# Performance work log

Hardware: AMD Instinct MI355X
Metric: run time of the kernel (lower is better)

The kernel has to match this reference:

```python
import jax, jax.numpy as jnp
import numpy as np

N = 100000        # num nodes
E = 3_200_000     # num edges
NFEAT, NHID, NCLASS = 256, 128, 40
BN_EPS = 1e-5


def _gcn_norm(edge_index, edge_weight, num_nodes):
    """PyG gcn_norm with self-loops (fill value 1.0): returns (src, dst, norm)."""
    loop = jnp.arange(num_nodes)
    src = jnp.concatenate([edge_index[0], loop])
    dst = jnp.concatenate([edge_index[1], loop])
    ew = jnp.concatenate([edge_weight, jnp.ones((num_nodes,), edge_weight.dtype)])
    deg = jax.ops.segment_sum(ew, dst, num_segments=num_nodes)
    dinv = jnp.where(deg > 0, jax.lax.rsqrt(jnp.maximum(deg, 1e-30)), 0.0)
    norm = dinv[src] * ew * dinv[dst]  # [E+N]
    return src, dst, norm


def _gcn_layer(h, W, b, src, dst, norm, num_nodes):
    lin = h @ W                                   # [N, out]
    msg = lin[src] * norm[:, None]                # gather + scale  [E+N, out]
    agg = jax.ops.segment_sum(msg, dst, num_segments=num_nodes)
    return agg + b


def _bn(h, gamma, beta):
    # BatchNorm1d in training mode: biased batch statistics
    m = jnp.mean(h, axis=0)
    v = jnp.mean(jnp.square(h - m), axis=0)
    return (h - m) * jax.lax.rsqrt(v + BN_EPS) * gamma + beta


def setup_inputs() -> dict:
    key = jax.random.key(0)
    ks = jax.random.split(key, 12)
    s_in = 1.0 / np.sqrt(NFEAT)
    s_h = 1.0 / np.sqrt(NHID)
    return {
        "x": jax.random.normal(ks[0], (N, NFEAT), jnp.float32),
        "edge_index": jax.random.randint(ks[1], (2, E), 0, N, dtype=jnp.int32),
        "edge_weight": jax.random.uniform(ks[2], (E,), jnp.float32),
        "W1": jax.random.normal(ks[3], (NFEAT, NHID), jnp.float32) * s_in,
        "b1": jnp.zeros((NHID,), jnp.float32),
        "g1": jnp.ones((NHID,), jnp.float32),
        "beta1": jnp.zeros((NHID,), jnp.float32),
        "W2": jax.random.normal(ks[4], (NHID, NHID), jnp.float32) * s_h,
        "b2": jnp.zeros((NHID,), jnp.float32),
        "g2": jnp.ones((NHID,), jnp.float32),
        "beta2": jnp.zeros((NHID,), jnp.float32),
        "W3": jax.random.normal(ks[5], (NHID, NHID), jnp.float32) * s_h,
        "b3": jnp.zeros((NHID,), jnp.float32),
        "g3": jnp.ones((NHID,), jnp.float32),
        "beta3": jnp.zeros((NHID,), jnp.float32),
        "linW": jax.random.normal(ks[6], (3 * NHID, NCLASS), jnp.float32) / np.sqrt(3 * NHID),
        "linb": jnp.zeros((NCLASS,), jnp.float32),
    }


def reference(x, edge_index, edge_weight,
              W1, b1, g1, beta1,
              W2, b2, g2, beta2,
              W3, b3, g3, beta3,
              linW, linb):
    src, dst, norm = _gcn_norm(edge_index, edge_weight, N)
    x1 = _bn(jax.nn.relu(_gcn_layer(x, W1, b1, src, dst, norm, N)), g1, beta1)
    x2 = _bn(jax.nn.relu(_gcn_layer(x1, W2, b2, src, dst, norm, N)), g2, beta2)
    x3 = _bn(_gcn_layer(x2, W3, b3, src, dst, norm, N), g3, beta3)  # note: no relu on x3
    embed_x = jnp.concatenate([x1, x2, x3], axis=1)  # [N, 3*NHID]
    logits = embed_x @ linW + linb                   # [N, NCLASS]
    return logits, jax.nn.softmax(logits, axis=1), embed_x
```

## Files before the change

### kernel.cpp

```cpp
#include <hip/hip_runtime.h>
#include <hip/hip_bf16.h>
#include <math.h>

#define NN 100000
#define NE 3200000
#define NF 256
#define NH 128
#define NC 40
#define BN_EPS 1e-5f

typedef __attribute__((ext_vector_type(8))) short bf16x8;
typedef __attribute__((ext_vector_type(4))) float f32x4;

__device__ __forceinline__ float2 bf2_unpack(unsigned int v) {
    return make_float2(__uint_as_float(v << 16), __uint_as_float(v & 0xffff0000u));
}
__device__ __forceinline__ unsigned int pack2bf(float lo, float hi) {
    unsigned int a = (unsigned int)__hip_bfloat16_raw(__float2bfloat16(lo)).x;
    unsigned int b = (unsigned int)__hip_bfloat16_raw(__float2bfloat16(hi)).x;
    return a | (b << 16);
}

__global__ __launch_bounds__(256) void k_init(unsigned long long* hist, float* sums) {
    int i = blockIdx.x * 256 + threadIdx.x;
    if (i < NN) hist[i] = 0ULL;
    if (i < 3 * 1024) sums[i] = 0.0f;
}

__global__ __launch_bounds__(256) void k_edge(const int* __restrict__ ei, const float* __restrict__ ew,
                                              unsigned long long* __restrict__ hist,
                                              int* __restrict__ pos) {
    int e = blockIdx.x * 256 + threadIdx.x;
    if (e >= NE) return;
    int d = ei[NE + e];
    float w = ew[e];
    unsigned long long pack = (1ULL << 44) | (unsigned long long)(w * 4294967296.0f);
    unsigned long long old = atomicAdd(&hist[d], pack);
    pos[e] = (int)(old >> 44);
}

__global__ __launch_bounds__(256) void k_dinv(const unsigned long long* __restrict__ hist,
                                              float* __restrict__ dinv) {
    int i = blockIdx.x * 256 + threadIdx.x;
    if (i < NN) {
        float ws = (float)(hist[i] & 0xFFFFFFFFFFFULL) * 2.3283064365386963e-10f;
        dinv[i] = rsqrtf(1.0f + ws);
    }
}

__global__ __launch_bounds__(1024) void k_scan(const unsigned long long* __restrict__ hist,
                                               int* __restrict__ rowptr) {
    __shared__ int wsum[16];
    __shared__ int s_carry;
    int t = threadIdx.x;
    int lane = t & 63, wid = t >> 6;
    if (t == 0) s_carry = 0;
    __syncthreads();
    for (int base = 0; base < NN; base += 4096) {
        int i0 = base + t * 4;
        int c[4];
#pragma unroll
        for (int j = 0; j < 4; j++) {
            int i = i0 + j;
            c[j] = (i < NN) ? (int)(hist[i] >> 44) : 0;
        }
        int v = c[0] + c[1] + c[2] + c[3];
        int x = v;
#pragma unroll
        for (int off = 1; off < 64; off <<= 1) {
            int y = __shfl_up(x, off);
            if (lane >= off) x += y;
        }
        if (lane == 63) wsum[wid] = x;
        __syncthreads();
        if (wid == 0 && lane < 16) {
            int s = wsum[lane];
#pragma unroll
            for (int off = 1; off < 16; off <<= 1) {
                int y = __shfl_up(s, off);
                if (lane >= off) s += y;
            }
            wsum[lane] = s;
        }
        __syncthreads();
        int woff = (wid > 0) ? wsum[wid - 1] : 0;
        int incl = x + woff;
        int carry = s_carry;
        int run = carry + incl - v;
#pragma unroll
        for (int j = 0; j < 4; j++) {
            int i = i0 + j;
            if (i < NN) rowptr[i] = run;
            run += c[j];
        }
        __syncthreads();
        if (t == 1023) s_carry = carry + incl;
        __syncthreads();
    }
    if (t == 0) rowptr[NN] = s_carry;
}

__global__ __launch_bounds__(256) void k_scatter(const int* __restrict__ ei, const float* __restrict__ ew,
                                                 const float* __restrict__ dinv,
                                                 const int* __restrict__ rowptr,
                                                 const int* __restrict__ pos,
                                                 int2* __restrict__ cw) {
    int e = blockIdx.x * 256 + threadIdx.x;
    if (e >= NE) return;
    int s = ei[e], d = ei[NE + e];
    float nv = dinv[s] * ew[e] * dinv[d];
    cw[rowptr[d] + pos[e]] = make_int2(s, __float_as_int(nv));
}

template <int K>
__global__ __launch_bounds__(256) void k_gemm_mfma(const float* __restrict__ H, int ldh,
                                                   const float* __restrict__ W,
                                                   __hip_bfloat16* __restrict__ out) {
    __shared__ unsigned int Bt[128][20];
    int t = threadIdx.x;
    int wid = t >> 6, l = t & 63;
    int l15 = l & 15, lhi = l >> 4;
    int rowbase = blockIdx.x * 128 + wid * 32;

    int ar0 = rowbase + l15;      if (ar0 >= NN) ar0 = NN - 1;
    int ar1 = rowbase + 16 + l15; if (ar1 >= NN) ar1 = NN - 1;

    f32x4 acc[2][8];
#pragma unroll
    for (int rt = 0; rt < 2; rt++)
#pragma unroll
        for (int ct = 0; ct < 8; ct++) acc[rt][ct] = (f32x4){0.f, 0.f, 0.f, 0.f};

    for (int kb = 0; kb < K / 32; kb++) {
        __syncthreads();
        for (int i = t; i < 2048; i += 256) {
            int c = i & 127, k2l = i >> 7;
            int k = kb * 32 + 2 * k2l;
            Bt[c][k2l] = pack2bf(W[(size_t)k * NH + c], W[(size_t)(k + 1) * NH + c]);
        }
        __syncthreads();
        const float4* a0p = (const float4*)&H[(size_t)ar0 * ldh + kb * 32 + lhi * 8];
        const float4* a1p = (const float4*)&H[(size_t)ar1 * ldh + kb * 32 + lhi * 8];
        float4 x0 = a0p[0], x1 = a0p[1];
        float4 y0 = a1p[0], y1 = a1p[1];
        union { unsigned int u[4]; bf16x8 v; } af0, af1;
        af0.u[0] = pack2bf(x0.x, x0.y); af0.u[1] = pack2bf(x0.z, x0.w);
        af0.u[2] = pack2bf(x1.x, x1.y); af0.u[3] = pack2bf(x1.z, x1.w);
        af1.u[0] = pack2bf(y0.x, y0.y); af1.u[1] = pack2bf(y0.z, y0.w);
        af1.u[2] = pack2bf(y1.x, y1.y); af1.u[3] = pack2bf(y1.z, y1.w);
#pragma unroll
        for (int ct = 0; ct < 8; ct++) {
            bf16x8 b = *(const bf16x8*)&Bt[ct * 16 + l15][lhi * 4];
            acc[0][ct] = __builtin_amdgcn_mfma_f32_16x16x32_bf16(af0.v, b, acc[0][ct], 0, 0, 0);
            acc[1][ct] = __builtin_amdgcn_mfma_f32_16x16x32_bf16(af1.v, b, acc[1][ct], 0, 0, 0);
        }
    }
#pragma unroll
    for (int rt = 0; rt < 2; rt++)
#pragma unroll
        for (int ct = 0; ct < 8; ct++)
#pragma unroll
            for (int reg = 0; reg < 4; reg++) {
                int row = rowbase + rt * 16 + lhi * 4 + reg;
                if (row < NN)
                    out[(size_t)row * NH + ct * 16 + l15] = __float2bfloat16(acc[rt][ct][reg]);
            }
}

__global__ __launch_bounds__(256) void k_agg(const unsigned int* __restrict__ linb,
                                             const float* __restrict__ dinv,
                                             const int* __restrict__ rowptr, const int2* __restrict__ cw,
                                             const float* __restrict__ bias,
                                             float* __restrict__ outp, int do_relu) {
    int t = threadIdx.x;
    int node = blockIdx.x * 4 + (t >> 6);
    if (node >= NN) return;
    int ch = t & 63;
    int c = ch << 1;
    float di = dinv[node];
    float2 sv = bf2_unpack(linb[(size_t)node * 64 + ch]);
    float a0 = fmaf(sv.x, di * di, bias[c]);
    float a1 = fmaf(sv.y, di * di, bias[c + 1]);
    int beg = rowptr[node], end = rowptr[node + 1];
    int j = beg;
    for (; j + 8 <= end; j += 8) {
        int2 p[8];
#pragma unroll
        for (int q = 0; q < 8; q++) p[q] = cw[j + q];
        unsigned int v[8];
#pragma unroll
        for (int q = 0; q < 8; q++) v[q] = linb[(size_t)(unsigned)p[q].x * 64 + ch];
#pragma unroll
        for (int q = 0; q < 8; q++) {
            float w = __int_as_float(p[q].y);
            float2 f = bf2_unpack(v[q]);
            a0 = fmaf(f.x, w, a0);
            a1 = fmaf(f.y, w, a1);
        }
    }
    for (; j < end; j++) {
        int2 p = cw[j];
        unsigned int vv = linb[(size_t)p.x * 64 + ch];
        float w = __int_as_float(p.y);
        float2 f = bf2_unpack(vv);
        a0 = fmaf(f.x, w, a0);
        a1 = fmaf(f.y, w, a1);
    }
    if (do_relu) { a0 = fmaxf(a0, 0.f); a1 = fmaxf(a1, 0.f); }
    *(float2*)&outp[(size_t)node * 384 + c] = make_float2(a0, a1);
}

__global__ __launch_bounds__(256) void k_stats(const float* __restrict__ pre, float* __restrict__ sums) {
    int t = threadIdx.x;
    int c = t & 127, h = t >> 7;
    float s = 0.f, s2 = 0.f;
    for (int r = blockIdx.x * 2 + h; r < NN; r += gridDim.x * 2) {
        float v = pre[(size_t)r * 384 + c];
        s += v;
        s2 = fmaf(v, v, s2);
    }
    __shared__ float ls[256], ls2[256];
    ls[t] = s; ls2[t] = s2;
    __syncthreads();
    if (t < 128) {
        atomicAdd(&sums[c], ls[t] + ls[t + 128]);
        atomicAdd(&sums[NH + c], ls2[t] + ls2[t + 128]);
    }
}

__global__ void k_bnfinal(float* __restrict__ sums, const float* __restrict__ g,
                          const float* __restrict__ beta) {
    int c = threadIdx.x;
    if (c < NH) {
        float m = sums[c] * (1.0f / NN);
        float v = sums[NH + c] * (1.0f / NN) - m * m;
        float rstd = rsqrtf(v + BN_EPS);
        float sc = g[c] * rstd;
        sums[256 + c] = sc;
        sums[384 + c] = beta[c] - m * sc;
    }
}

__global__ __launch_bounds__(256) void k_bnapply(float* __restrict__ pre, const float* __restrict__ sums) {
    int idx = blockIdx.x * 256 + threadIdx.x;
    if (idx >= NN * 64) return;
    int n = idx >> 6, cp = (idx & 63) << 1;
    float2 sc = *(const float2*)&sums[256 + cp];
    float2 sh = *(const float2*)&sums[384 + cp];
    float2 v = *(float2*)&pre[(size_t)n * 384 + cp];
    v.x = fmaf(v.x, sc.x, sh.x);
    v.y = fmaf(v.y, sc.y, sh.y);
    *(float2*)&pre[(size_t)n * 384 + cp] = v;
}

__global__ __launch_bounds__(256) void k_final(const float* __restrict__ embed,
                                               const float* __restrict__ linW,
                                               const float* __restrict__ linb,
                                               float* __restrict__ logits, float* __restrict__ probs) {
    __shared__ unsigned int Wt[3 * 16 * 196];
    int t = threadIdx.x;
    for (int i = t; i < 3 * 16 * 192; i += 256) {
        int ct = i / (16 * 192);
        int rem = i - ct * (16 * 192);
        int c = rem / 192, k2 = rem - c * 192;
        int col = ct * 16 + c;
        float lo = (col < NC) ? linW[(size_t)(2 * k2) * NC + col] : 0.f;
        float hi = (col < NC) ? linW[(size_t)(2 * k2 + 1) * NC + col] : 0.f;
        Wt[(ct * 16 + c) * 196 + k2] = pack2bf(lo, hi);
    }
    __syncthreads();

    int wid = t >> 6, l = t & 63;
    int rowbase = blockIdx.x * 64 + wid * 16;
    int l15 = l & 15, lhi = l >> 4;

    int arow = rowbase + l15;
    if (arow > NN - 1) arow = NN - 1;
    const float4* ap = (const float4*)&embed[(size_t)arow * 384 + lhi * 8];

    f32x4 acc0 = {0.f, 0.f, 0.f, 0.f};
    f32x4 acc1 = {0.f, 0.f, 0.f, 0.f};
    f32x4 acc2 = {0.f, 0.f, 0.f, 0.f};

    for (int kb = 0; kb < 12; kb++) {
        float4 a0 = ap[kb * 8];
        float4 a1 = ap[kb * 8 + 1];
        union { unsigned int u[4]; bf16x8 v; } af;
        af.u[0] = pack2bf(a0.x, a0.y);
        af.u[1] = pack2bf(a0.z, a0.w);
        af.u[2] = pack2bf(a1.x, a1.y);
        af.u[3] = pack2bf(a1.z, a1.w);
        int wbase = kb * 16 + lhi * 4;
        bf16x8 b0 = *(const bf16x8*)&Wt[(0 * 16 + l15) * 196 + wbase];
        bf16x8 b1 = *(const bf16x8*)&Wt[(1 * 16 + l15) * 196 + wbase];
        bf16x8 b2 = *(const bf16x8*)&Wt[(2 * 16 + l15) * 196 + wbase];
        acc0 = __builtin_amdgcn_mfma_f32_16x16x32_bf16(af.v, b0, acc0, 0, 0, 0);
        acc1 = __builtin_amdgcn_mfma_f32_16x16x32_bf16(af.v, b1, acc1, 0, 0, 0);
        acc2 = __builtin_amdgcn_mfma_f32_16x16x32_bf16(af.v, b2, acc2, 0, 0, 0);
    }

    int col0 = 0 * 16 + l15, col1 = 1 * 16 + l15, col2 = 2 * 16 + l15;
    float lb0 = (col0 < NC) ? linb[col0] : 0.f;
    float lb1 = (col1 < NC) ? linb[col1] : 0.f;
    float lb2 = (col2 < NC) ? linb[col2] : 0.f;

#pragma unroll
    for (int reg = 0; reg < 4; reg++) {
        int row = rowbase + lhi * 4 + reg;
        float v0 = acc0[reg] + lb0;
        float v1 = acc1[reg] + lb1;
        float v2 = acc2[reg] + lb2;
        float m = fmaxf(v0, v1);
        if (col2 < NC) m = fmaxf(m, v2);
#pragma unroll
        for (int off = 1; off < 16; off <<= 1) m = fmaxf(m, __shfl_xor(m, off));
        float e0 = __expf(v0 - m);
        float e1 = __expf(v1 - m);
        float e2 = (col2 < NC) ? __expf(v2 - m) : 0.f;
        float s = e0 + e1 + e2;
#pragma unroll
        for (int off = 1; off < 16; off <<= 1) s += __shfl_xor(s, off);
        float inv = 1.0f / s;
        if (row < NN) {
            size_t base = (size_t)row * NC;
            logits[base + col0] = v0;
            probs[base + col0] = e0 * inv;
            logits[base + col1] = v1;
            probs[base + col1] = e1 * inv;
            if (col2 < NC) {
                logits[base + col2] = v2;
                probs[base + col2] = e2 * inv;
            }
        }
    }
}

extern "C" void kernel_launch(void* const* d_in, const int* in_sizes, int n_in,
                              void* d_out, int out_size, void* d_ws, size_t ws_size,
                              hipStream_t stream) {
    const float* x    = (const float*)d_in[0];
    const int*   ei   = (const int*)d_in[1];
    const float* ew   = (const float*)d_in[2];
    const float* W1   = (const float*)d_in[3];
    const float* b1   = (const float*)d_in[4];
    const float* g1   = (const float*)d_in[5];
    const float* be1  = (const float*)d_in[6];
    const float* W2   = (const float*)d_in[7];
    const float* b2   = (const float*)d_in[8];
    const float* g2   = (const float*)d_in[9];
    const float* be2  = (const float*)d_in[10];
    const float* W3   = (const float*)d_in[11];
    const float* b3   = (const float*)d_in[12];
    const float* g3   = (const float*)d_in[13];
    const float* be3  = (const float*)d_in[14];
    const float* linW = (const float*)d_in[15];
    const float* linb = (const float*)d_in[16];

    float* out    = (float*)d_out;
    float* logits = out;
    float* probs  = out + (size_t)NN * NC;
    float* embed  = out + (size_t)2 * NN * NC;

    char* ws = (char*)d_ws;
    size_t off = 0;
    auto alloc = [&](size_t bytes) -> char* {
        char* p = ws + off;
        off = (off + bytes + 255) & ~(size_t)255;
        return p;
    };
    float*              dinv   = (float*)alloc((size_t)NN * 4);
    unsigned long long* hist   = (unsigned long long*)alloc((size_t)NN * 8);
    int*                rowptr = (int*)alloc((size_t)(NN + 1) * 4);
    int2*               cw     = (int2*)alloc((size_t)NE * 8);
    __hip_bfloat16*     lin    = (__hip_bfloat16*)alloc((size_t)NN * NH * 2);
    float*              sums   = (float*)alloc(3 * 1024 * 4);
    int*                pos    = (int*)lin;
    (void)ws_size; (void)in_sizes; (void)n_in; (void)out_size;

    int gN = (NN + 255) / 256;
    int gE = (NE + 255) / 256;
    int gM = (NN + 127) / 128;
    int gA = (NN + 3) / 4;
    int gB = (NN * 64 + 255) / 256;
    int gF = (NN + 63) / 64;

    k_init<<<gN, 256, 0, stream>>>(hist, sums);
    k_edge<<<gE, 256, 0, stream>>>(ei, ew, hist, pos);
    k_dinv<<<gN, 256, 0, stream>>>(hist, dinv);
    k_scan<<<1, 1024, 0, stream>>>(hist, rowptr);
    k_scatter<<<gE, 256, 0, stream>>>(ei, ew, dinv, rowptr, pos, cw);

    k_gemm_mfma<NF><<<gM, 256, 0, stream>>>(x, NF, W1, lin);
    k_agg<<<gA, 256, 0, stream>>>((const unsigned int*)lin, dinv, rowptr, cw, b1, embed + 0, 1);
    k_stats<<<1024, 256, 0, stream>>>(embed + 0, sums + 0);
    k_bnfinal<<<1, 128, 0, stream>>>(sums + 0, g1, be1);
    k_bnapply<<<gB, 256, 0, stream>>>(embed + 0, sums + 0);
    k_gemm_mfma<NH><<<gM, 256, 0, stream>>>(embed + 0, 384, W2, lin);
    k_agg<<<gA, 256, 0, stream>>>((const unsigned int*)lin, dinv, rowptr, cw, b2, embed + 128, 1);
    k_stats<<<1024, 256, 0, stream>>>(embed + 128, sums + 1024);
    k_bnfinal<<<1, 128, 0, stream>>>(sums + 1024, g2, be2);
    k_bnapply<<<gB, 256, 0, stream>>>(embed + 128, sums + 1024);
    k_gemm_mfma<NH><<<gM, 256, 0, stream>>>(embed + 128, 384, W3, lin);
    k_agg<<<gA, 256, 0, stream>>>((const unsigned int*)lin, dinv, rowptr, cw, b3, embed + 256, 0);
    k_stats<<<1024, 256, 0, stream>>>(embed + 256, sums + 2048);
    k_bnfinal<<<1, 128, 0, stream>>>(sums + 2048, g3, be3);
    k_bnapply<<<gB, 256, 0, stream>>>(embed + 256, sums + 2048);
    k_final<<<gF, 256, 0, stream>>>(embed, linW, linb, logits, probs);
}
```

Before: 1.066 ms.

## Fuse BN stats into aggregation, pack CSR edges to 32 bits, vectorize BN apply

Each edge entry is packed into one 32-bit word: a 17-bit source index plus a 15-bit positive fp16 weight. This halves the CSR traffic read by every aggregation pass. The aggregation kernel becomes grid-stride with a fixed grid and accumulates the per-channel sum and sum of squares, so the separate stats pass over the embedding goes away. The edge and scatter kernels gain nontemporal loads and stores, and bnapply is widened to float4. Storing weights in fp16 costs precision, and the packing relies on node indices fitting in 17 bits.

```diff
diff --git a/kernel.cpp b/kernel.cpp
--- a/kernel.cpp
+++ b/kernel.cpp
@@ -1,5 +1,6 @@
 #include <hip/hip_runtime.h>
 #include <hip/hip_bf16.h>
+#include <hip/hip_fp16.h>
 #include <math.h>
 
 #define NN 100000
@@ -32,11 +33,11 @@
                                               int* __restrict__ pos) {
     int e = blockIdx.x * 256 + threadIdx.x;
     if (e >= NE) return;
-    int d = ei[NE + e];
-    float w = ew[e];
+    int d = __builtin_nontemporal_load(&ei[NE + e]);
+    float w = __builtin_nontemporal_load(&ew[e]);
     unsigned long long pack = (1ULL << 44) | (unsigned long long)(w * 4294967296.0f);
     unsigned long long old = atomicAdd(&hist[d], pack);
-    pos[e] = (int)(old >> 44);
+    __builtin_nontemporal_store((int)(old >> 44), &pos[e]);
 }
 
 __global__ __launch_bounds__(256) void k_dinv(const unsigned long long* __restrict__ hist,
@@ -104,12 +105,17 @@
                                                  const float* __restrict__ dinv,
                                                  const int* __restrict__ rowptr,
                                                  const int* __restrict__ pos,
-                                                 int2* __restrict__ cw) {
+                                                 unsigned int* __restrict__ cw) {
     int e = blockIdx.x * 256 + threadIdx.x;
     if (e >= NE) return;
-    int s = ei[e], d = ei[NE + e];
-    float nv = dinv[s] * ew[e] * dinv[d];
-    cw[rowptr[d] + pos[e]] = make_int2(s, __float_as_int(nv));
+    int s = __builtin_nontemporal_load(&ei[e]);
+    int d = __builtin_nontemporal_load(&ei[NE + e]);
+    float w = __builtin_nontemporal_load(&ew[e]);
+    float nv = dinv[s] * w * dinv[d];
+    unsigned int h = (unsigned int)__half_as_ushort(__float2half(nv)) & 0x7fffu;
+    unsigned int packed = (unsigned int)s | (h << 17);
+    int p = __builtin_nontemporal_load(&pos[e]);
+    __builtin_nontemporal_store(packed, &cw[rowptr[d] + p]);
 }
 
 template <int K>
@@ -169,62 +175,66 @@
 
 __global__ __launch_bounds__(256) void k_agg(const unsigned int* __restrict__ linb,
                                              const float* __restrict__ dinv,
-                                             const int* __restrict__ rowptr, const int2* __restrict__ cw,
+                                             const int* __restrict__ rowptr,
+                                             const unsigned int* __restrict__ cw,
                                              const float* __restrict__ bias,
-                                             float* __restrict__ outp, int do_relu) {
+                                             float* __restrict__ outp,
+                                             float* __restrict__ sums, int do_relu) {
     int t = threadIdx.x;
-    int node = blockIdx.x * 4 + (t >> 6);
-    if (node >= NN) return;
-    int ch = t & 63;
+    int wid = t >> 6, ch = t & 63;
     int c = ch << 1;
-    float di = dinv[node];
-    float2 sv = bf2_unpack(linb[(size_t)node * 64 + ch]);
-    float a0 = fmaf(sv.x, di * di, bias[c]);
-    float a1 = fmaf(sv.y, di * di, bias[c + 1]);
-    int beg = rowptr[node], end = rowptr[node + 1];
-    int j = beg;
-    for (; j + 8 <= end; j += 8) {
-        int2 p[8];
-#pragma unroll
-        for (int q = 0; q < 8; q++) p[q] = cw[j + q];
-        unsigned int v[8];
-#pragma unroll
-        for (int q = 0; q < 8; q++) v[q] = linb[(size_t)(unsigned)p[q].x * 64 + ch];
-#pragma unroll
-        for (int q = 0; q < 8; q++) {
-            float w = __int_as_float(p[q].y);
-            float2 f = bf2_unpack(v[q]);
+    float bb0 = bias[c], bb1 = bias[c + 1];
+    float s0 = 0.f, s1 = 0.f, q0 = 0.f, q1 = 0.f;
+    for (int node = blockIdx.x * 4 + wid; node < NN; node += gridDim.x * 4) {
+        float di = dinv[node];
+        float2 sv = bf2_unpack(linb[(size_t)node * 64 + ch]);
+        float a0 = fmaf(sv.x, di * di, bb0);
+        float a1 = fmaf(sv.y, di * di, bb1);
+        int beg = rowptr[node], end = rowptr[node + 1];
+        int j = beg;
+        for (; j + 8 <= end; j += 8) {
+            unsigned int pk[8];
+#pragma unroll
+            for (int q = 0; q < 8; q++) pk[q] = __builtin_nontemporal_load(&cw[j + q]);
+            unsigned int v[8];
+#pragma unroll
+            for (int q = 0; q < 8; q++) v[q] = linb[(size_t)(pk[q] & 0x1FFFFu) * 64 + ch];
+#pragma unroll
+            for (int q = 0; q < 8; q++) {
+                float w = __half2float(__ushort_as_half((unsigned short)(pk[q] >> 17)));
+                float2 f = bf2_unpack(v[q]);
+                a0 = fmaf(f.x, w, a0);
+                a1 = fmaf(f.y, w, a1);
+            }
+        }
+        for (; j < end; j++) {
+            unsigned int pk = __builtin_nontemporal_load(&cw[j]);
+            unsigned int vv = linb[(size_t)(pk & 0x1FFFFu) * 64 + ch];
+            float w = __half2float(__ushort_as_half((unsigned short)(pk >> 17)));
+            float2 f = bf2_unpack(vv);
             a0 = fmaf(f.x, w, a0);
             a1 = fmaf(f.y, w, a1);
         }
-    }
-    for (; j < end; j++) {
-        int2 p = cw[j];
-        unsigned int vv = linb[(size_t)p.x * 64 + ch];
-        float w = __int_as_float(p.y);
-        float2 f = bf2_unpack(vv);
-        a0 = fmaf(f.x, w, a0);
-        a1 = fmaf(f.y, w, a1);
-    }
-    if (do_relu) { a0 = fmaxf(a0, 0.f); a1 = fmaxf(a1, 0.f); }
-    *(float2*)&outp[(size_t)node * 384 + c] = make_float2(a0, a1);
-}
-
-__global__ __launch_bounds__(256) void k_stats(const float* __restrict__ pre, float* __restrict__ sums) {
-    int t = threadIdx.x;
-    int c = t & 127, h = t >> 7;
-    float s = 0.f, s2 = 0.f;
-    for (int r = blockIdx.x * 2 + h; r < NN; r += gridDim.x * 2) {
-        float v = pre[(size_t)r * 384 + c];
-        s += v;
-        s2 = fmaf(v, v, s2);
-    }
-    __shared__ float ls[256], ls2[256];
-    ls[t] = s; ls2[t] = s2;
+        if (do_relu) { a0 = fmaxf(a0, 0.f); a1 = fmaxf(a1, 0.f); }
+        *(float2*)&outp[(size_t)node * 384 + c] = make_float2(a0, a1);
+        s0 += a0; s1 += a1;
+        q0 = fmaf(a0, a0, q0); q1 = fmaf(a1, a1, q1);
+    }
+    __shared__ float red[4][64][4];
+    red[wid][ch][0] = s0; red[wid][ch][1] = s1;
+    red[wid][ch][2] = q0; red[wid][ch][3] = q1;
     __syncthreads();
-    if (t < 128) {
-        atomicAdd(&sums[c], ls[t] + ls[t + 128]);
-        atomicAdd(&sums[NH + c], ls2[t] + ls2[t + 128]);
+    if (t < 64) {
+        float S0 = 0.f, S1 = 0.f, Q0 = 0.f, Q1 = 0.f;
+#pragma unroll
+        for (int w2 = 0; w2 < 4; w2++) {
+            S0 += red[w2][t][0]; S1 += red[w2][t][1];
+            Q0 += red[w2][t][2]; Q1 += red[w2][t][3];
+        }
+        atomicAdd(&sums[2 * t], S0);
+        atomicAdd(&sums[2 * t + 1], S1);
+        atomicAdd(&sums[NH + 2 * t], Q0);
+        atomicAdd(&sums[NH + 2 * t + 1], Q1);
     }
 }
 
@@ -243,14 +253,16 @@
 
 __global__ __launch_bounds__(256) void k_bnapply(float* __restrict__ pre, const float* __restrict__ sums) {
     int idx = blockIdx.x * 256 + threadIdx.x;
-    if (idx >= NN * 64) return;
-    int n = idx >> 6, cp = (idx & 63) << 1;
-    float2 sc = *(const float2*)&sums[256 + cp];
-    float2 sh = *(const float2*)&sums[384 + cp];
-    float2 v = *(float2*)&pre[(size_t)n * 384 + cp];
+    if (idx >= NN * 32) return;
+    int n = idx >> 5, cp = (idx & 31) << 2;
+    float4 sc = *(const float4*)&sums[256 + cp];
+    float4 sh = *(const float4*)&sums[384 + cp];
+    float4 v = *(float4*)&pre[(size_t)n * 384 + cp];
     v.x = fmaf(v.x, sc.x, sh.x);
     v.y = fmaf(v.y, sc.y, sh.y);
-    *(float2*)&pre[(size_t)n * 384 + cp] = v;
+    v.z = fmaf(v.z, sc.z, sh.z);
+    v.w = fmaf(v.w, sc.w, sh.w);
+    *(float4*)&pre[(size_t)n * 384 + cp] = v;
 }
 
 __global__ __launch_bounds__(256) void k_final(const float* __restrict__ embed,
@@ -371,7 +383,7 @@
     float*              dinv   = (float*)alloc((size_t)NN * 4);
     unsigned long long* hist   = (unsigned long long*)alloc((size_t)NN * 8);
     int*                rowptr = (int*)alloc((size_t)(NN + 1) * 4);
-    int2*               cw     = (int2*)alloc((size_t)NE * 8);
+    unsigned int*       cw     = (unsigned int*)alloc((size_t)NE * 4);
     __hip_bfloat16*     lin    = (__hip_bfloat16*)alloc((size_t)NN * NH * 2);
     float*              sums   = (float*)alloc(3 * 1024 * 4);
     int*                pos    = (int*)lin;
@@ -380,9 +392,9 @@
     int gN = (NN + 255) / 256;
     int gE = (NE + 255) / 256;
     int gM = (NN + 127) / 128;
-    int gA = (NN + 3) / 4;
-    int gB = (NN * 64 + 255) / 256;
+    int gB = (NN * 32 + 255) / 256;
     int gF = (NN + 63) / 64;
+    int gA = 2048;
 
     k_init<<<gN, 256, 0, stream>>>(hist, sums);
     k_edge<<<gE, 256, 0, stream>>>(ei, ew, hist, pos);
@@ -391,18 +403,15 @@
     k_scatter<<<gE, 256, 0, stream>>>(ei, ew, dinv, rowptr, pos, cw);
 
     k_gemm_mfma<NF><<<gM, 256, 0, stream>>>(x, NF, W1, lin);
-    k_agg<<<gA, 256, 0, stream>>>((const unsigned int*)lin, dinv, rowptr, cw, b1, embed + 0, 1);
-    k_stats<<<1024, 256, 0, stream>>>(embed + 0, sums + 0);
+    k_agg<<<gA, 256, 0, stream>>>((const unsigned int*)lin, dinv, rowptr, cw, b1, embed + 0, sums + 0, 1);
     k_bnfinal<<<1, 128, 0, stream>>>(sums + 0, g1, be1);
     k_bnapply<<<gB, 256, 0, stream>>>(embed + 0, sums + 0);
     k_gemm_mfma<NH><<<gM, 256, 0, stream>>>(embed + 0, 384, W2, lin);
-    k_agg<<<gA, 256, 0, stream>>>((const unsigned int*)lin, dinv, rowptr, cw, b2, embed + 128, 1);
-    k_stats<<<1024, 256, 0, stream>>>(embed + 128, sums + 1024);
+    k_agg<<<gA, 256, 0, stream>>>((const unsigned int*)lin, dinv, rowptr, cw, b2, embed + 128, sums + 1024, 1);
     k_bnfinal<<<1, 128, 0, stream>>>(sums + 1024, g2, be2);
     k_bnapply<<<gB, 256, 0, stream>>>(embed + 128, sums + 1024);
     k_gemm_mfma<NH><<<gM, 256, 0, stream>>>(embed + 128, 384, W3, lin);
-    k_agg<<<gA, 256, 0, stream>>>((const unsigned int*)lin, dinv, rowptr, cw, b3, embed + 256, 0);
-    k_stats<<<1024, 256, 0, stream>>>(embed + 256, sums + 2048);
+    k_agg<<<gA, 256, 0, stream>>>((const unsigned int*)lin, dinv, rowptr, cw, b3, embed + 256, sums + 2048, 0);
     k_bnfinal<<<1, 128, 0, stream>>>(sums + 2048, g3, be3);
     k_bnapply<<<gB, 256, 0, stream>>>(embed + 256, sums + 2048);
     k_final<<<gF, 256, 0, stream>>>(embed, linW, linb, logits, probs);
```

Result: slower. 1.211 ms (+13.6%).

## Pack CSR entries into 32 bits with fp16 weights; widen agg unroll and bnapply

Applied to the files above, without the earlier changes.

Each CSR entry is packed into one 32-bit word: a 17-bit source index plus a 15-bit fp16 normalized weight with the sign bit dropped. This halves the edge-list traffic read by the three aggregation passes. The aggregation loop is also unrolled to 16 with a 4-wide tail, BN apply moves to float4, and non-temporal loads and stores are used in the edge preprocessing kernels. The cost is lower weight precision, and the packing assumes node ids fit in 17 bits and weights are non-negative.

```diff
diff --git a/kernel.cpp b/kernel.cpp
--- a/kernel.cpp
+++ b/kernel.cpp
@@ -1,5 +1,6 @@
 #include <hip/hip_runtime.h>
 #include <hip/hip_bf16.h>
+#include <hip/hip_fp16.h>
 #include <math.h>
 
 #define NN 100000
@@ -32,11 +33,11 @@
                                               int* __restrict__ pos) {
     int e = blockIdx.x * 256 + threadIdx.x;
     if (e >= NE) return;
-    int d = ei[NE + e];
-    float w = ew[e];
+    int d = __builtin_nontemporal_load(&ei[NE + e]);
+    float w = __builtin_nontemporal_load(&ew[e]);
     unsigned long long pack = (1ULL << 44) | (unsigned long long)(w * 4294967296.0f);
     unsigned long long old = atomicAdd(&hist[d], pack);
-    pos[e] = (int)(old >> 44);
+    __builtin_nontemporal_store((int)(old >> 44), &pos[e]);
 }
 
 __global__ __launch_bounds__(256) void k_dinv(const unsigned long long* __restrict__ hist,
@@ -104,12 +105,17 @@
                                                  const float* __restrict__ dinv,
                                                  const int* __restrict__ rowptr,
                                                  const int* __restrict__ pos,
-                                                 int2* __restrict__ cw) {
+                                                 unsigned int* __restrict__ cw) {
     int e = blockIdx.x * 256 + threadIdx.x;
     if (e >= NE) return;
-    int s = ei[e], d = ei[NE + e];
-    float nv = dinv[s] * ew[e] * dinv[d];
-    cw[rowptr[d] + pos[e]] = make_int2(s, __float_as_int(nv));
+    int s = __builtin_nontemporal_load(&ei[e]);
+    int d = __builtin_nontemporal_load(&ei[NE + e]);
+    float w = __builtin_nontemporal_load(&ew[e]);
+    float nv = dinv[s] * w * dinv[d];
+    unsigned int h = (unsigned int)__half_as_ushort(__float2half(nv)) & 0x7fffu;
+    unsigned int packed = (unsigned int)s | (h << 17);
+    int p = __builtin_nontemporal_load(&pos[e]);
+    __builtin_nontemporal_store(packed, &cw[rowptr[d] + p]);
 }
 
 template <int K>
@@ -169,7 +175,8 @@
 
 __global__ __launch_bounds__(256) void k_agg(const unsigned int* __restrict__ linb,
                                              const float* __restrict__ dinv,
-                                             const int* __restrict__ rowptr, const int2* __restrict__ cw,
+                                             const int* __restrict__ rowptr,
+                                             const unsigned int* __restrict__ cw,
                                              const float* __restrict__ bias,
                                              float* __restrict__ outp, int do_relu) {
     int t = threadIdx.x;
@@ -183,25 +190,40 @@
     float a1 = fmaf(sv.y, di * di, bias[c + 1]);
     int beg = rowptr[node], end = rowptr[node + 1];
     int j = beg;
-    for (; j + 8 <= end; j += 8) {
-        int2 p[8];
-#pragma unroll
-        for (int q = 0; q < 8; q++) p[q] = cw[j + q];
-        unsigned int v[8];
-#pragma unroll
-        for (int q = 0; q < 8; q++) v[q] = linb[(size_t)(unsigned)p[q].x * 64 + ch];
-#pragma unroll
-        for (int q = 0; q < 8; q++) {
-            float w = __int_as_float(p[q].y);
+    for (; j + 16 <= end; j += 16) {
+        unsigned int pk[16];
+#pragma unroll
+        for (int q = 0; q < 16; q++) pk[q] = cw[j + q];
+        unsigned int v[16];
+#pragma unroll
+        for (int q = 0; q < 16; q++) v[q] = linb[(size_t)(pk[q] & 0x1FFFFu) * 64 + ch];
+#pragma unroll
+        for (int q = 0; q < 16; q++) {
+            float w = __half2float(__ushort_as_half((unsigned short)(pk[q] >> 17)));
             float2 f = bf2_unpack(v[q]);
             a0 = fmaf(f.x, w, a0);
             a1 = fmaf(f.y, w, a1);
         }
     }
+    for (; j + 4 <= end; j += 4) {
+        unsigned int pk[4];
+#pragma unroll
+        for (int q = 0; q < 4; q++) pk[q] = cw[j + q];
+        unsigned int v[4];
+#pragma unroll
+        for (int q = 0; q < 4; q++) v[q] = linb[(size_t)(pk[q] & 0x1FFFFu) * 64 + ch];
+#pragma unroll
+        for (int q = 0; q < 4; q++) {
+            float w = __half2float(__ushort_as_half((unsigned short)(pk[q] >> 17)));
+            float2 f = bf2_unpack(v[q]);
+            a0 = fmaf(f.x, w, a0);
+            a1 = fmaf(f.y, w, a1);
+        }
+    }
     for (; j < end; j++) {
-        int2 p = cw[j];
-        unsigned int vv = linb[(size_t)p.x * 64 + ch];
-        float w = __int_as_float(p.y);
+        unsigned int pk = cw[j];
+        unsigned int vv = linb[(size_t)(pk & 0x1FFFFu) * 64 + ch];
+        float w = __half2float(__ushort_as_half((unsigned short)(pk >> 17)));
         float2 f = bf2_unpack(vv);
         a0 = fmaf(f.x, w, a0);
         a1 = fmaf(f.y, w, a1);
@@ -243,14 +265,16 @@
 
 __global__ __launch_bounds__(256) void k_bnapply(float* __restrict__ pre, const float* __restrict__ sums) {
     int idx = blockIdx.x * 256 + threadIdx.x;
-    if (idx >= NN * 64) return;
-    int n = idx >> 6, cp = (idx & 63) << 1;
-    float2 sc = *(const float2*)&sums[256 + cp];
-    float2 sh = *(const float2*)&sums[384 + cp];
-    float2 v = *(float2*)&pre[(size_t)n * 384 + cp];
+    if (idx >= NN * 32) return;
+    int n = idx >> 5, cp = (idx & 31) << 2;
+    float4 sc = *(const float4*)&sums[256 + cp];
+    float4 sh = *(const float4*)&sums[384 + cp];
+    float4 v = *(float4*)&pre[(size_t)n * 384 + cp];
     v.x = fmaf(v.x, sc.x, sh.x);
     v.y = fmaf(v.y, sc.y, sh.y);
-    *(float2*)&pre[(size_t)n * 384 + cp] = v;
+    v.z = fmaf(v.z, sc.z, sh.z);
+    v.w = fmaf(v.w, sc.w, sh.w);
+    *(float4*)&pre[(size_t)n * 384 + cp] = v;
 }
 
 __global__ __launch_bounds__(256) void k_final(const float* __restrict__ embed,
@@ -371,7 +395,7 @@
     float*              dinv   = (float*)alloc((size_t)NN * 4);
     unsigned long long* hist   = (unsigned long long*)alloc((size_t)NN * 8);
     int*                rowptr = (int*)alloc((size_t)(NN + 1) * 4);
-    int2*               cw     = (int2*)alloc((size_t)NE * 8);
+    unsigned int*       cw     = (unsigned int*)alloc((size_t)NE * 4);
     __hip_bfloat16*     lin    = (__hip_bfloat16*)alloc((size_t)NN * NH * 2);
     float*              sums   = (float*)alloc(3 * 1024 * 4);
     int*                pos    = (int*)lin;
@@ -381,7 +405,7 @@
     int gE = (NE + 255) / 256;
     int gM = (NN + 127) / 128;
     int gA = (NN + 3) / 4;
-    int gB = (NN * 64 + 255) / 256;
+    int gB = (NN * 32 + 255) / 256;
     int gF = (NN + 63) / 64;
 
     k_init<<<gN, 256, 0, stream>>>(hist, sums);
```

Result: faster. 1.030 ms (-3.4%).
